# Performance work log

Measured on AMD Instinct MI355X. Metric: run time of the kernel, lower is better.

Reference implementation:

```python
import jax, jax.numpy as jnp
import numpy as np

DIM = 10
ITERATIONS = 2
N_NODES = 500_000
N_EDGES = 8_000_000


def _linear(x, W, b):
    # torch nn.Linear: y = x @ W.T + b
    return x @ W.T + b


def setup_inputs() -> dict:
    key = jax.random.key(0)
    ks = jax.random.split(key, 16)
    inp = {
        "h": jax.random.normal(ks[0], (N_NODES, DIM), dtype=jnp.float32),
        "edges": jax.random.randint(ks[1], (2, N_EDGES), 0, N_NODES, dtype=jnp.int64)
        if jax.config.jax_enable_x64
        else jax.random.randint(ks[1], (2, N_EDGES), 0, N_NODES, dtype=jnp.int32),
        "depth": jax.random.randint(ks[2], (N_NODES,), 0, 4, dtype=jnp.int32),
    }
    names = ["Wz", "bz", "Uz", "buz", "Wr", "br", "Ur", "bur", "Wh", "bh", "Uh", "buh"]
    s = 1.0 / np.sqrt(DIM)
    for i, n in enumerate(names):
        shape = (DIM, DIM) if n[0] in ("W", "U") else (DIM,)
        inp[n] = jax.random.uniform(ks[3 + i], shape, jnp.float32, -s, s)
    return inp


def reference(h, edges, depth, Wz, bz, Uz, buz, Wr, br, Ur, bur, Wh, bh, Uh, buh):
    recv, send = edges[0], edges[1]
    for i in range(ITERATIONS):
        active = (depth + i) <= ITERATIONS                      # [N] bool, shrinks with i
        h = jnp.where(active[:, None], h, 0.0)                  # drop inactive nodes (dict-key drop)
        # x[u] = sum over edges (u,v) with v active of h[v]; h already zeroed for inactive v
        x = jax.ops.segment_sum(h[send], recv, num_segments=h.shape[0])  # [N, DIM]
        z = jax.nn.sigmoid(_linear(x, Wz, bz) + _linear(h, Uz, buz))
        r = jax.nn.sigmoid(_linear(x, Wr, br) + _linear(h, Ur, bur))
        h_new = z * h + (1.0 - z) * jnp.tanh(_linear(x, Wh, bh) + _linear(r * h, Uh, buh))
        h = jnp.where(active[:, None], h_new, 0.0)
    return h
```

## Files before the change

### kernel.cpp

```cpp
#include <hip/hip_runtime.h>
#include <hip/hip_fp16.h>
#include <math.h>
#include <stdint.h>

#define DIM 10
#define NTILE 256
#define BKT_LOG 8
#define BKT 256
#define NBMAX 2048
#define EPW 2048
#define KPT (EPW / 256)
#define CAPB 2816
#define CAPF 1280
#define CAPK (CAPB - CAPF)
#define OVFCAP 32768
#define D2WORDS 32768


__device__ __forceinline__ float2 cvt2(uint32_t u) {
    __half2 hh = *reinterpret_cast<__half2*>(&u);
    return __half22float2(hh);
}

__device__ __forceinline__ int d2get(const uint32_t* __restrict__ depth2, int node) {
    uint32_t w = depth2[(uint32_t)node >> 4];
    return (int)((w >> ((node & 15) * 2)) & 3u);
}

__global__ void prep_kernel(const int* __restrict__ depth,
                            uint32_t* __restrict__ depth2,
                            uint32_t* __restrict__ cnts,
                            int n, int pack_blocks, int cnt_tot)
{
    __shared__ int sd[4096];
    const int t = threadIdx.x;
    const int bid = blockIdx.x;
    if (bid < pack_blocks) {
        const int base = bid * 4096;
        for (int i = t; i < 4096; i += 256) {
            int g = base + i;
            sd[i] = (g < n) ? depth[g] : 3;
        }
        __syncthreads();
        const int wbase = base >> 4;
        int wb = wbase + t;
        if (wb * 16 < n) {
            uint32_t v = 0;
            #pragma unroll
            for (int j = 0; j < 16; ++j)
                v |= ((uint32_t)(sd[t * 16 + j] & 3)) << (2 * j);
            depth2[wb] = v;
        }
    } else {
        int i = (bid - pack_blocks) * 256 + t;
        if (i < cnt_tot) cnts[i] = 0;
    }
}

__global__ __launch_bounds__(256) void binit_kernel(
                           const int* __restrict__ recv,
                           const int* __restrict__ send,
                           const uint32_t* __restrict__ depth2,
                           const int* __restrict__ depth,
                           const float* __restrict__ h_in,
                           uint16_t* __restrict__ h16a,
                           uint32_t* __restrict__ cntF,
                           uint32_t* __restrict__ cntB,
                           uint32_t* __restrict__ ovfc,
                           uint32_t* __restrict__ ovf,
                           uint32_t* __restrict__ bins,
                           int ne, int n, int bin_blocks)
{
    __shared__ uint32_t u[3 * NBMAX];
    const int t = threadIdx.x;
    const int bid = blockIdx.x;

    if (bid < bin_blocks) {
        uint32_t* lh  = u;
        uint32_t* wgF = u + NBMAX;
        uint32_t* wgB = u + 2 * NBMAX;
        for (int i = t; i < NBMAX; i += 256) lh[i] = 0;
        __syncthreads();

        const int base = bid * EPW;
        int rA[KPT], sA[KPT];
        #pragma unroll
        for (int k = 0; k < KPT; ++k) {
            int e = base + k * 256 + t;
            if (e < ne) { rA[k] = recv[e]; sA[k] = send[e]; }
            else        { rA[k] = -1;      sA[k] = 0;       }
        }
        int drA[KPT], dsA[KPT];
        #pragma unroll
        for (int k = 0; k < KPT; ++k) {
            if (rA[k] >= 0) { drA[k] = d2get(depth2, rA[k]); dsA[k] = d2get(depth2, sA[k]); }
            else            { drA[k] = 3;                    dsA[k] = 3;                    }
        }
        uint32_t fl = 0;
        #pragma unroll
        for (int k = 0; k < KPT; ++k) {
            if (rA[k] >= 0 && drA[k] <= 2 && dsA[k] <= 2) {
                bool f1 = (drA[k] <= 1) && (dsA[k] <= 1);
                fl |= (f1 ? 3u : 1u) << (2 * k);
                atomicAdd(&lh[rA[k] >> BKT_LOG], f1 ? 1u : 0x10000u);
            }
        }
        __syncthreads();

        for (int i = t; i < NBMAX; i += 256) {
            uint32_t v = lh[i];
            if (v) {
                uint32_t f = v & 0xffffu, kb = v >> 16;
                if (f)  wgF[i] = atomicAdd(&cntF[i], f);
                if (kb) wgB[i] = atomicAdd(&cntB[i], kb);
            }
        }
        __syncthreads();
        for (int i = t; i < NBMAX; i += 256) lh[i] = 0;
        __syncthreads();

        #pragma unroll
        for (int k = 0; k < KPT; ++k) {
            if ((fl >> (2 * k)) & 1u) {
                int r = rA[k], s = sA[k];
                int b = r >> BKT_LOG;
                bool f1 = (fl >> (2 * k)) & 2u;
                uint32_t w = (uint32_t)s | ((uint32_t)(r & (BKT - 1)) << 19)
                           | (f1 ? (1u << 27) : 0u);
                if (f1) {
                    uint32_t o = atomicAdd(&lh[b], 1u) & 0xffffu;
                    uint32_t pos = wgF[b] + o;
                    if (pos < CAPF) bins[(size_t)b * CAPB + pos] = w;
                    else { uint32_t oi = atomicAdd(ovfc, 1u);
                           if (oi < OVFCAP) ovf[oi] = (uint32_t)(base + k * 256 + t); }
                } else {
                    uint32_t o = atomicAdd(&lh[b], 0x10000u) >> 16;
                    uint32_t pos = wgB[b] + o;
                    if (pos < CAPK) bins[(size_t)b * CAPB + (CAPB - 1) - pos] = w;
                    else { uint32_t oi = atomicAdd(ovfc, 1u);
                           if (oi < OVFCAP) ovf[oi] = (uint32_t)(base + k * 256 + t); }
                }
            }
        }
    } else {
        float* sh = reinterpret_cast<float*>(u);
        const int tile = bid - bin_blocks;
        const int base = tile * NTILE;

        const long gbase = (long)base * DIM;
        const long glim  = (long)n * DIM;
        for (int idx = t; idx < NTILE * DIM; idx += NTILE) {
            long g = gbase + idx;
            float v = (g < glim) ? h_in[g] : 0.0f;
            sh[(idx / DIM) * 11 + (idx % DIM)] = v;
        }
        __syncthreads();

        const int node = base + t;
        if (node < n && depth[node] > 2) {
            #pragma unroll
            for (int c = 0; c < DIM; ++c) sh[t * 11 + c] = 0.0f;
        }
        __syncthreads();

        uint32_t* o16 = reinterpret_cast<uint32_t*>(h16a);
        const long o16base = (long)base * 8;
        const long o16lim  = (long)n * 8;
        for (int idx = t; idx < NTILE * 8; idx += NTILE) {
            long g = o16base + idx;
            if (g < o16lim) {
                int nl = idx / 8, c2 = idx % 8;
                uint32_t w = 0;
                if (c2 < 5) {
                    __half2 hh = __floats2half2_rn(sh[nl * 11 + 2 * c2],
                                                   sh[nl * 11 + 2 * c2 + 1]);
                    w = *reinterpret_cast<uint32_t*>(&hh);
                }
                o16[g] = w;
            }
        }
    }
}

template<int ITER>
__global__ __launch_bounds__(256, 6) void scatgru_kernel(
                            const uint32_t* __restrict__ bins,
                            const uint32_t* __restrict__ cntF,
                            const uint32_t* __restrict__ cntB,
                            const uint32_t* __restrict__ ovfc,
                            const uint32_t* __restrict__ ovf,
                            const int* __restrict__ recv,
                            const int* __restrict__ send,
                            const int* __restrict__ depth,
                            const uint16_t* __restrict__ hcur,
                            uint16_t* __restrict__ hnext,
                            float* __restrict__ out32,
                            int n,
                            const float* __restrict__ Wz, const float* __restrict__ bz,
                            const float* __restrict__ Uz, const float* __restrict__ buz,
                            const float* __restrict__ Wr, const float* __restrict__ br,
                            const float* __restrict__ Ur, const float* __restrict__ bur,
                            const float* __restrict__ Wh, const float* __restrict__ bh,
                            const float* __restrict__ Uh, const float* __restrict__ buh)
{
    __shared__ float xl[BKT * DIM];
    __shared__ float sW[6][100];
    __shared__ float sb[3][10];

    const int t = threadIdx.x;
    if (t < 100) {
        sW[0][t] = Wz[t]; sW[1][t] = Uz[t];
        sW[2][t] = Wr[t]; sW[3][t] = Ur[t];
        sW[4][t] = Wh[t]; sW[5][t] = Uh[t];
    }
    if (t < 10) {
        sb[0][t] = bz[t] + buz[t];
        sb[1][t] = br[t] + bur[t];
        sb[2][t] = bh[t] + buh[t];
    }
    for (int i = t; i < BKT * DIM; i += 256) xl[i] = 0.0f;
    __syncthreads();

    const int b = blockIdx.x;
    const int n0 = b << BKT_LOG;
    const int nb = min(BKT, n - n0);

    const size_t base = (size_t)b * CAPB;
    const int fc = (int)min(cntF[b], (uint32_t)CAPF);
    int tot = fc, boff = 0;
    if (ITER == 0) {
        int bc = (int)min(cntB[b], (uint32_t)CAPK);
        tot = fc + bc;
        boff = CAPB - bc - fc;
    }

    for (int i = t; i < tot; i += 256) {
        size_t idx = base + (size_t)((ITER == 0 && i >= fc) ? (i + boff) : i);
        uint32_t w = bins[idx];
        size_t s = (size_t)(w & 0x7FFFFu);
        uint4 q = *reinterpret_cast<const uint4*>(hcur + s * 16);
        uint32_t e8 = *reinterpret_cast<const uint32_t*>(hcur + s * 16 + 8);
        float2 f0 = cvt2(q.x), f1 = cvt2(q.y), f2 = cvt2(q.z), f3 = cvt2(q.w);
        float2 f4 = cvt2(e8);
        float* xr = xl + ((w >> 19) & (BKT - 1)) * DIM;
        atomicAdd(xr + 0, f0.x); atomicAdd(xr + 1, f0.y);
        atomicAdd(xr + 2, f1.x); atomicAdd(xr + 3, f1.y);
        atomicAdd(xr + 4, f2.x); atomicAdd(xr + 5, f2.y);
        atomicAdd(xr + 6, f3.x); atomicAdd(xr + 7, f3.y);
        atomicAdd(xr + 8, f4.x); atomicAdd(xr + 9, f4.y);
    }

    {
        const uint32_t cnt = min(*ovfc, (uint32_t)OVFCAP);
        for (uint32_t i = t; i < cnt; i += 256) {
            int e = (int)ovf[i];
            int r = recv[e];
            if ((r >> BKT_LOG) != b) continue;
            int s = send[e];
            if (ITER == 1 && (depth[r] > 1 || depth[s] > 1)) continue;
            uint4 q = *reinterpret_cast<const uint4*>(hcur + (size_t)s * 16);
            uint32_t e8v = *reinterpret_cast<const uint32_t*>(hcur + (size_t)s * 16 + 8);
            float2 f0 = cvt2(q.x), f1 = cvt2(q.y), f2 = cvt2(q.z), f3 = cvt2(q.w);
            float2 f4 = cvt2(e8v);
            float* xr = xl + (r & (BKT - 1)) * DIM;
            atomicAdd(xr + 0, f0.x); atomicAdd(xr + 1, f0.y);
            atomicAdd(xr + 2, f1.x); atomicAdd(xr + 3, f1.y);
            atomicAdd(xr + 4, f2.x); atomicAdd(xr + 5, f2.y);
            atomicAdd(xr + 6, f3.x); atomicAdd(xr + 7, f3.y);
            atomicAdd(xr + 8, f4.x); atomicAdd(xr + 9, f4.y);
        }
    }
    __syncthreads();

    if (t < nb) {
        const int node = n0 + t;
        const int dep = depth[node];
        const bool active = (dep + ITER) <= 2;

        float hv[DIM];
        {
            const uint16_t* hp = hcur + (size_t)node * 16;
            uint4 q = *reinterpret_cast<const uint4*>(hp);
            uint32_t e8v = *reinterpret_cast<const uint32_t*>(hp + 8);
            float2 f0 = cvt2(q.x), f1 = cvt2(q.y), f2 = cvt2(q.z), f3 = cvt2(q.w);
            float2 f4 = cvt2(e8v);
            hv[0] = f0.x; hv[1] = f0.y; hv[2] = f1.x; hv[3] = f1.y;
            hv[4] = f2.x; hv[5] = f2.y; hv[6] = f3.x; hv[7] = f3.y;
            hv[8] = f4.x; hv[9] = f4.y;
        }
        float xv[DIM];
        #pragma unroll
        for (int j = 0; j < DIM; ++j) xv[j] = xl[t * DIM + j];

        float zz[DIM];
        if (active) {
            #pragma unroll
            for (int i = 0; i < DIM; ++i) {
                float az = sb[0][i];
                float ar = sb[1][i];
                #pragma unroll
                for (int j = 0; j < DIM; ++j) {
                    az = fmaf(xv[j], sW[0][i * DIM + j], az);
                    az = fmaf(hv[j], sW[1][i * DIM + j], az);
                    ar = fmaf(xv[j], sW[2][i * DIM + j], ar);
                    ar = fmaf(hv[j], sW[3][i * DIM + j], ar);
                }
                zz[i] = 1.0f / (1.0f + __expf(-az));
                xl[t * DIM + i] = (1.0f / (1.0f + __expf(-ar))) * hv[i];
            }
        }

        if (ITER == 0) {
            uint32_t packed[5];
            float prev = 0.0f;
            #pragma unroll
            for (int i = 0; i < DIM; ++i) {
                float o;
                if (active) {
                    float ah = sb[2][i];
                    #pragma unroll
                    for (int j = 0; j < DIM; ++j) {
                        ah = fmaf(xv[j], sW[4][i * DIM + j], ah);
                        ah = fmaf(xl[t * DIM + j], sW[5][i * DIM + j], ah);
                    }
                    o = zz[i] * hv[i] + (1.0f - zz[i]) * tanhf(ah);
                } else {
                    o = hv[i];
                }
                if (dep > 1) o = 0.0f;
                if (i & 1) {
                    __half2 hh = __floats2half2_rn(prev, o);
                    packed[i >> 1] = *reinterpret_cast<uint32_t*>(&hh);
                } else prev = o;
            }
            uint4 o0 = make_uint4(packed[0], packed[1], packed[2], packed[3]);
            uint4 o1 = make_uint4(packed[4], 0u, 0u, 0u);
            *reinterpret_cast<uint4*>(hnext + (size_t)node * 16)     = o0;
            *reinterpret_cast<uint4*>(hnext + (size_t)node * 16 + 8) = o1;
        } else {
            float2* op = reinterpret_cast<float2*>(out32 + (size_t)node * DIM);
            float prev = 0.0f;
            #pragma unroll
            for (int i = 0; i < DIM; ++i) {
                float o;
                if (active) {
                    float ah = sb[2][i];
                    #pragma unroll
                    for (int j = 0; j < DIM; ++j) {
                        ah = fmaf(xv[j], sW[4][i * DIM + j], ah);
                        ah = fmaf(xl[t * DIM + j], sW[5][i * DIM + j], ah);
                    }
                    o = zz[i] * hv[i] + (1.0f - zz[i]) * tanhf(ah);
                } else {
                    o = hv[i];
                }
                if (i & 1) op[i >> 1] = make_float2(prev, o);
                else prev = o;
            }
        }
    }
}

__global__ void init_mask32_kernel(const float* __restrict__ hsrc,
                                   float* __restrict__ hdst,
                                   const int* __restrict__ depth,
                                   int n)
{
    int node = blockIdx.x * blockDim.x + threadIdx.x;
    if (node >= n) return;
    bool act = depth[node] <= 2;
    const float* s = hsrc + (size_t)node * DIM;
    float* d = hdst + (size_t)node * DIM;
    #pragma unroll
    for (int c = 0; c < DIM; ++c) d[c] = act ? s[c] : 0.0f;
}

__global__ void simple_scatter_kernel(const int* __restrict__ recv,
                                      const int* __restrict__ send,
                                      const float* __restrict__ hm,
                                      float* __restrict__ x,
                                      int ne)
{
    const int tid = blockIdx.x * blockDim.x + threadIdx.x;
    const int e = tid / DIM;
    if (e >= ne) return;
    const int c = tid - e * DIM;
    const int s = send[e];
    const float v = hm[(size_t)s * DIM + c];
    if (v != 0.0f) {
        const int r = recv[e];
        unsafeAtomicAdd(x + (size_t)r * DIM + c, v);
    }
}

__global__ void zero_buf_kernel(float4* __restrict__ p, int tot4) {
    int i = blockIdx.x * blockDim.x + threadIdx.x;
    if (i < tot4) p[i] = make_float4(0.0f, 0.0f, 0.0f, 0.0f);
}

__global__ void gru32_kernel(const float* __restrict__ x,
                             const float* __restrict__ h,
                             float* __restrict__ out,
                             const int* __restrict__ depth, int iter, int n,
                             const float* __restrict__ Wz, const float* __restrict__ bz,
                             const float* __restrict__ Uz, const float* __restrict__ buz,
                             const float* __restrict__ Wr, const float* __restrict__ br,
                             const float* __restrict__ Ur, const float* __restrict__ bur,
                             const float* __restrict__ Wh, const float* __restrict__ bh,
                             const float* __restrict__ Uh, const float* __restrict__ buh)
{
    __shared__ float sW[6][100];
    __shared__ float sb[3][10];
    const int t = threadIdx.x;
    if (t < 100) {
        sW[0][t] = Wz[t]; sW[1][t] = Uz[t];
        sW[2][t] = Wr[t]; sW[3][t] = Ur[t];
        sW[4][t] = Wh[t]; sW[5][t] = Uh[t];
    }
    if (t < 10) {
        sb[0][t] = bz[t] + buz[t];
        sb[1][t] = br[t] + bur[t];
        sb[2][t] = bh[t] + buh[t];
    }
    __syncthreads();

    int node = blockIdx.x * blockDim.x + t;
    if (node >= n) return;
    const int dep = depth[node];
    const bool active = dep + iter <= 2;
    float xv[DIM], hv[DIM], outv[DIM];
    #pragma unroll
    for (int j = 0; j < DIM; ++j) {
        xv[j] = x[(size_t)node * DIM + j];
        hv[j] = h[(size_t)node * DIM + j];
    }
    if (active) {
        float zz[DIM], rr[DIM];
        #pragma unroll
        for (int i = 0; i < DIM; ++i) {
            float az = sb[0][i], ar = sb[1][i];
            #pragma unroll
            for (int j = 0; j < DIM; ++j) {
                az = fmaf(xv[j], sW[0][i * DIM + j], az);
                az = fmaf(hv[j], sW[1][i * DIM + j], az);
                ar = fmaf(xv[j], sW[2][i * DIM + j], ar);
                ar = fmaf(hv[j], sW[3][i * DIM + j], ar);
            }
            zz[i] = 1.0f / (1.0f + __expf(-az));
            rr[i] = 1.0f / (1.0f + __expf(-ar));
        }
        float rh[DIM];
        #pragma unroll
        for (int j = 0; j < DIM; ++j) rh[j] = rr[j] * hv[j];
        #pragma unroll
        for (int i = 0; i < DIM; ++i) {
            float ah = sb[2][i];
            #pragma unroll
            for (int j = 0; j < DIM; ++j) {
                ah = fmaf(xv[j], sW[4][i * DIM + j], ah);
                ah = fmaf(rh[j], sW[5][i * DIM + j], ah);
            }
            outv[i] = zz[i] * hv[i] + (1.0f - zz[i]) * tanhf(ah);
        }
    } else {
        #pragma unroll
        for (int i = 0; i < DIM; ++i) outv[i] = hv[i];
    }
    if (iter == 0 && dep > 1) {
        #pragma unroll
        for (int i = 0; i < DIM; ++i) outv[i] = 0.0f;
    }
    #pragma unroll
    for (int i = 0; i < DIM; ++i) out[(size_t)node * DIM + i] = outv[i];
}

extern "C" void kernel_launch(void* const* d_in, const int* in_sizes, int n_in,
                              void* d_out, int out_size, void* d_ws, size_t ws_size,
                              hipStream_t stream) {
    const float* h_in  = (const float*)d_in[0];
    const int*   edges = (const int*)d_in[1];
    const int*   depth = (const int*)d_in[2];
    const float* Wz  = (const float*)d_in[3];
    const float* bz  = (const float*)d_in[4];
    const float* Uz  = (const float*)d_in[5];
    const float* buz = (const float*)d_in[6];
    const float* Wr  = (const float*)d_in[7];
    const float* br  = (const float*)d_in[8];
    const float* Ur  = (const float*)d_in[9];
    const float* bur = (const float*)d_in[10];
    const float* Wh  = (const float*)d_in[11];
    const float* bh  = (const float*)d_in[12];
    const float* Uh  = (const float*)d_in[13];
    const float* buh = (const float*)d_in[14];

    const int n  = in_sizes[0] / DIM;
    const int ne = in_sizes[1] / 2;
    const int* recv = edges;
    const int* send = edges + ne;

    const int NB = (n + BKT - 1) >> BKT_LOG;
    const size_t meta_words = 2 * NBMAX + 8 + OVFCAP + D2WORDS;
    const size_t need = (size_t)n * 16 * sizeof(uint16_t) * 2
                      + (size_t)NB * CAPB * sizeof(uint32_t)
                      + meta_words * sizeof(uint32_t);

    const int BLK = 256;

    if (ws_size >= need && n <= (1 << 19) && NB <= NBMAX) {
        uint16_t* h16a = (uint16_t*)d_ws;
        uint16_t* h16b = h16a + (size_t)n * 16;
        uint32_t* bins = (uint32_t*)(h16b + (size_t)n * 16);
        uint32_t* meta = bins + (size_t)NB * CAPB;
        uint32_t* cntF   = meta;
        uint32_t* cntB   = meta + NBMAX;
        uint32_t* ovfc   = meta + 2 * NBMAX;
        uint32_t* ovf    = meta + 2 * NBMAX + 8;
        uint32_t* depth2 = meta + 2 * NBMAX + 8 + OVFCAP;

        const int bin_blocks  = (ne + EPW - 1) / EPW;
        const int node_blocks = (n + NTILE - 1) / NTILE;
        const int pack_blocks = (n + 4095) / 4096;
        const int cnt_tot = 2 * NBMAX + 1;
        const int cnt_blocks = (cnt_tot + 255) / 256;

        prep_kernel<<<pack_blocks + cnt_blocks, BLK, 0, stream>>>(
            depth, depth2, meta, n, pack_blocks, cnt_tot);
        binit_kernel<<<bin_blocks + node_blocks, BLK, 0, stream>>>(
            recv, send, depth2, depth, h_in, h16a,
            cntF, cntB, ovfc, ovf, bins, ne, n, bin_blocks);

        scatgru_kernel<0><<<NB, BLK, 0, stream>>>(
            bins, cntF, cntB, ovfc, ovf, recv, send, depth,
            h16a, h16b, nullptr, n,
            Wz, bz, Uz, buz, Wr, br, Ur, bur, Wh, bh, Uh, buh);

        scatgru_kernel<1><<<NB, BLK, 0, stream>>>(
            bins, cntF, cntB, ovfc, ovf, recv, send, depth,
            h16b, nullptr, (float*)d_out, n,
            Wz, bz, Uz, buz, Wr, br, Ur, bur, Wh, bh, Uh, buh);
    } else {
        float* x    = (float*)d_ws;
        float* hbuf = (float*)d_out;
        const int nwork = ne * DIM;
        const int edge_blocks = (nwork + BLK - 1) / BLK;
        const int x_tot4 = (n * DIM) / 4;
        const int xz_blocks = (x_tot4 + BLK - 1) / BLK;
        const int nb2 = (n + BLK - 1) / BLK;

        init_mask32_kernel<<<nb2, BLK, 0, stream>>>(h_in, hbuf, depth, n);
        zero_buf_kernel<<<xz_blocks, BLK, 0, stream>>>((float4*)x, x_tot4);
        simple_scatter_kernel<<<edge_blocks, BLK, 0, stream>>>(recv, send, hbuf, x, ne);
        gru32_kernel<<<nb2, BLK, 0, stream>>>(x, hbuf, hbuf, depth, 0, n,
            Wz, bz, Uz, buz, Wr, br, Ur, bur, Wh, bh, Uh, buh);
        zero_buf_kernel<<<xz_blocks, BLK, 0, stream>>>((float4*)x, x_tot4);
        simple_scatter_kernel<<<edge_blocks, BLK, 0, stream>>>(recv, send, hbuf, x, ne);
        gru32_kernel<<<nb2, BLK, 0, stream>>>(x, hbuf, hbuf, depth, 1, n,
            Wz, bz, Uz, buz, Wr, br, Ur, bur, Wh, bh, Uh, buh);
    }
}
```

Baseline: 554.7 us.

## Replace two-pass block-aggregated binning with sender-partitioned direct atomic bins

The edge binning drops the per-block shared-memory histogram and two-phase offset reservation. Each edge now does a direct global atomicAdd into a cell keyed by (sender partition, receiver bucket), with 8 partitions of capacity 448. The per-bucket GRU kernel walks partitions in order so gathered sender rows are more localized, and in iteration 1 it filters out non-f1 edges by a flag bit instead of using a separate bin region. It also pads the shared x accumulator stride to 11 to cut LDS bank conflicts and raises the occupancy hint. The trade is many more global atomics with higher contention, and a higher overflow risk from the smaller per-cell capacity.

```diff
diff --git a/kernel.cpp b/kernel.cpp
--- a/kernel.cpp
+++ b/kernel.cpp
@@ -10,11 +10,12 @@
 #define NBMAX 2048
 #define EPW 2048
 #define KPT (EPW / 256)
-#define CAPB 2816
-#define CAPF 1280
-#define CAPK (CAPB - CAPF)
+#define NPART 8
+#define PSHIFT 16
+#define CAP 448
 #define OVFCAP 32768
 #define D2WORDS 32768
+#define XSTR 11
 
 
 __device__ __forceinline__ float2 cvt2(uint32_t u) {
@@ -42,8 +43,7 @@
             sd[i] = (g < n) ? depth[g] : 3;
         }
         __syncthreads();
-        const int wbase = base >> 4;
-        int wb = wbase + t;
+        int wb = (base >> 4) + t;
         if (wb * 16 < n) {
             uint32_t v = 0;
             #pragma unroll
@@ -64,24 +64,17 @@
                            const int* __restrict__ depth,
                            const float* __restrict__ h_in,
                            uint16_t* __restrict__ h16a,
-                           uint32_t* __restrict__ cntF,
-                           uint32_t* __restrict__ cntB,
+                           uint32_t* __restrict__ cnt,
                            uint32_t* __restrict__ ovfc,
                            uint32_t* __restrict__ ovf,
                            uint32_t* __restrict__ bins,
-                           int ne, int n, int bin_blocks)
+                           int ne, int n, int NB, int bin_blocks)
 {
-    __shared__ uint32_t u[3 * NBMAX];
+    __shared__ float sh[NTILE * 11];
     const int t = threadIdx.x;
     const int bid = blockIdx.x;
 
     if (bid < bin_blocks) {
-        uint32_t* lh  = u;
-        uint32_t* wgF = u + NBMAX;
-        uint32_t* wgB = u + 2 * NBMAX;
-        for (int i = t; i < NBMAX; i += 256) lh[i] = 0;
-        __syncthreads();
-
         const int base = bid * EPW;
         int rA[KPT], sA[KPT];
         #pragma unroll
@@ -96,57 +89,22 @@
             if (rA[k] >= 0) { drA[k] = d2get(depth2, rA[k]); dsA[k] = d2get(depth2, sA[k]); }
             else            { drA[k] = 3;                    dsA[k] = 3;                    }
         }
-        uint32_t fl = 0;
         #pragma unroll
         for (int k = 0; k < KPT; ++k) {
             if (rA[k] >= 0 && drA[k] <= 2 && dsA[k] <= 2) {
+                int r = rA[k], s = sA[k];
                 bool f1 = (drA[k] <= 1) && (dsA[k] <= 1);
-                fl |= (f1 ? 3u : 1u) << (2 * k);
-                atomicAdd(&lh[rA[k] >> BKT_LOG], f1 ? 1u : 0x10000u);
-            }
-        }
-        __syncthreads();
-
-        for (int i = t; i < NBMAX; i += 256) {
-            uint32_t v = lh[i];
-            if (v) {
-                uint32_t f = v & 0xffffu, kb = v >> 16;
-                if (f)  wgF[i] = atomicAdd(&cntF[i], f);
-                if (kb) wgB[i] = atomicAdd(&cntB[i], kb);
-            }
-        }
-        __syncthreads();
-        for (int i = t; i < NBMAX; i += 256) lh[i] = 0;
-        __syncthreads();
-
-        #pragma unroll
-        for (int k = 0; k < KPT; ++k) {
-            if ((fl >> (2 * k)) & 1u) {
-                int r = rA[k], s = sA[k];
-                int b = r >> BKT_LOG;
-                bool f1 = (fl >> (2 * k)) & 2u;
                 uint32_t w = (uint32_t)s | ((uint32_t)(r & (BKT - 1)) << 19)
                            | (f1 ? (1u << 27) : 0u);
-                if (f1) {
-                    uint32_t o = atomicAdd(&lh[b], 1u) & 0xffffu;
-                    uint32_t pos = wgF[b] + o;
-                    if (pos < CAPF) bins[(size_t)b * CAPB + pos] = w;
-                    else { uint32_t oi = atomicAdd(ovfc, 1u);
-                           if (oi < OVFCAP) ovf[oi] = (uint32_t)(base + k * 256 + t); }
-                } else {
-                    uint32_t o = atomicAdd(&lh[b], 0x10000u) >> 16;
-                    uint32_t pos = wgB[b] + o;
-                    if (pos < CAPK) bins[(size_t)b * CAPB + (CAPB - 1) - pos] = w;
-                    else { uint32_t oi = atomicAdd(ovfc, 1u);
-                           if (oi < OVFCAP) ovf[oi] = (uint32_t)(base + k * 256 + t); }
-                }
+                int cell = (s >> PSHIFT) * NB + (r >> BKT_LOG);
+                uint32_t pos = atomicAdd(&cnt[cell], 1u);
+                if (pos < CAP) bins[(size_t)cell * CAP + pos] = w;
+                else { uint32_t oi = atomicAdd(ovfc, 1u);
+                       if (oi < OVFCAP) ovf[oi] = (uint32_t)(base + k * 256 + t); }
             }
         }
     } else {
-        float* sh = reinterpret_cast<float*>(u);
-        const int tile = bid - bin_blocks;
-        const int base = tile * NTILE;
-
+        const int base = (bid - bin_blocks) * NTILE;
         const long gbase = (long)base * DIM;
         const long glim  = (long)n * DIM;
         for (int idx = t; idx < NTILE * DIM; idx += NTILE) {
@@ -155,14 +113,12 @@
             sh[(idx / DIM) * 11 + (idx % DIM)] = v;
         }
         __syncthreads();
-
         const int node = base + t;
         if (node < n && depth[node] > 2) {
             #pragma unroll
             for (int c = 0; c < DIM; ++c) sh[t * 11 + c] = 0.0f;
         }
         __syncthreads();
-
         uint32_t* o16 = reinterpret_cast<uint32_t*>(h16a);
         const long o16base = (long)base * 8;
         const long o16lim  = (long)n * 8;
@@ -183,10 +139,9 @@
 }
 
 template<int ITER>
-__global__ __launch_bounds__(256, 6) void scatgru_kernel(
+__global__ __launch_bounds__(256, 8) void scatgru_kernel(
                             const uint32_t* __restrict__ bins,
-                            const uint32_t* __restrict__ cntF,
-                            const uint32_t* __restrict__ cntB,
+                            const uint32_t* __restrict__ cnt,
                             const uint32_t* __restrict__ ovfc,
                             const uint32_t* __restrict__ ovf,
                             const int* __restrict__ recv,
@@ -195,7 +150,7 @@
                             const uint16_t* __restrict__ hcur,
                             uint16_t* __restrict__ hnext,
                             float* __restrict__ out32,
-                            int n,
+                            int n, int NB,
                             const float* __restrict__ Wz, const float* __restrict__ bz,
                             const float* __restrict__ Uz, const float* __restrict__ buz,
                             const float* __restrict__ Wr, const float* __restrict__ br,
@@ -203,7 +158,7 @@
                             const float* __restrict__ Wh, const float* __restrict__ bh,
                             const float* __restrict__ Uh, const float* __restrict__ buh)
 {
-    __shared__ float xl[BKT * DIM];
+    __shared__ float xl[BKT * XSTR];
     __shared__ float sW[6][100];
     __shared__ float sb[3][10];
 
@@ -218,41 +173,37 @@
         sb[1][t] = br[t] + bur[t];
         sb[2][t] = bh[t] + buh[t];
     }
-    for (int i = t; i < BKT * DIM; i += 256) xl[i] = 0.0f;
+    for (int i = t; i < BKT * XSTR; i += 256) xl[i] = 0.0f;
     __syncthreads();
 
     const int b = blockIdx.x;
     const int n0 = b << BKT_LOG;
     const int nb = min(BKT, n - n0);
 
-    const size_t base = (size_t)b * CAPB;
-    const int fc = (int)min(cntF[b], (uint32_t)CAPF);
-    int tot = fc, boff = 0;
-    if (ITER == 0) {
-        int bc = (int)min(cntB[b], (uint32_t)CAPK);
-        tot = fc + bc;
-        boff = CAPB - bc - fc;
-    }
-
-    for (int i = t; i < tot; i += 256) {
-        size_t idx = base + (size_t)((ITER == 0 && i >= fc) ? (i + boff) : i);
-        uint32_t w = bins[idx];
-        size_t s = (size_t)(w & 0x7FFFFu);
-        uint4 q = *reinterpret_cast<const uint4*>(hcur + s * 16);
-        uint32_t e8 = *reinterpret_cast<const uint32_t*>(hcur + s * 16 + 8);
-        float2 f0 = cvt2(q.x), f1 = cvt2(q.y), f2 = cvt2(q.z), f3 = cvt2(q.w);
-        float2 f4 = cvt2(e8);
-        float* xr = xl + ((w >> 19) & (BKT - 1)) * DIM;
-        atomicAdd(xr + 0, f0.x); atomicAdd(xr + 1, f0.y);
-        atomicAdd(xr + 2, f1.x); atomicAdd(xr + 3, f1.y);
-        atomicAdd(xr + 4, f2.x); atomicAdd(xr + 5, f2.y);
-        atomicAdd(xr + 6, f3.x); atomicAdd(xr + 7, f3.y);
-        atomicAdd(xr + 8, f4.x); atomicAdd(xr + 9, f4.y);
+    for (int p = 0; p < NPART; ++p) {
+        const int cell = p * NB + b;
+        const size_t base = (size_t)cell * CAP;
+        const int tot = (int)min(cnt[cell], (uint32_t)CAP);
+        for (int i = t; i < tot; i += 256) {
+            uint32_t w = bins[base + i];
+            if (ITER == 1 && !((w >> 27) & 1u)) continue;
+            size_t s = (size_t)(w & 0x7FFFFu);
+            uint4 q = *reinterpret_cast<const uint4*>(hcur + s * 16);
+            uint32_t e8 = *reinterpret_cast<const uint32_t*>(hcur + s * 16 + 8);
+            float2 f0 = cvt2(q.x), f1 = cvt2(q.y), f2 = cvt2(q.z), f3 = cvt2(q.w);
+            float2 f4 = cvt2(e8);
+            float* xr = xl + ((w >> 19) & (BKT - 1)) * XSTR;
+            atomicAdd(xr + 0, f0.x); atomicAdd(xr + 1, f0.y);
+            atomicAdd(xr + 2, f1.x); atomicAdd(xr + 3, f1.y);
+            atomicAdd(xr + 4, f2.x); atomicAdd(xr + 5, f2.y);
+            atomicAdd(xr + 6, f3.x); atomicAdd(xr + 7, f3.y);
+            atomicAdd(xr + 8, f4.x); atomicAdd(xr + 9, f4.y);
+        }
     }
 
     {
-        const uint32_t cnt = min(*ovfc, (uint32_t)OVFCAP);
-        for (uint32_t i = t; i < cnt; i += 256) {
+        const uint32_t cntv = min(*ovfc, (uint32_t)OVFCAP);
+        for (uint32_t i = t; i < cntv; i += 256) {
             int e = (int)ovf[i];
             int r = recv[e];
             if ((r >> BKT_LOG) != b) continue;
@@ -262,7 +213,7 @@
             uint32_t e8v = *reinterpret_cast<const uint32_t*>(hcur + (size_t)s * 16 + 8);
             float2 f0 = cvt2(q.x), f1 = cvt2(q.y), f2 = cvt2(q.z), f3 = cvt2(q.w);
             float2 f4 = cvt2(e8v);
-            float* xr = xl + (r & (BKT - 1)) * DIM;
+            float* xr = xl + (r & (BKT - 1)) * XSTR;
             atomicAdd(xr + 0, f0.x); atomicAdd(xr + 1, f0.y);
             atomicAdd(xr + 2, f1.x); atomicAdd(xr + 3, f1.y);
             atomicAdd(xr + 4, f2.x); atomicAdd(xr + 5, f2.y);
@@ -290,7 +241,7 @@
         }
         float xv[DIM];
         #pragma unroll
-        for (int j = 0; j < DIM; ++j) xv[j] = xl[t * DIM + j];
+        for (int j = 0; j < DIM; ++j) xv[j] = xl[t * XSTR + j];
 
         float zz[DIM];
         if (active) {
@@ -306,7 +257,7 @@
                     ar = fmaf(hv[j], sW[3][i * DIM + j], ar);
                 }
                 zz[i] = 1.0f / (1.0f + __expf(-az));
-                xl[t * DIM + i] = (1.0f / (1.0f + __expf(-ar))) * hv[i];
+                xl[t * XSTR + i] = (1.0f / (1.0f + __expf(-ar))) * hv[i];
             }
         }
 
@@ -321,7 +272,7 @@
                     #pragma unroll
                     for (int j = 0; j < DIM; ++j) {
                         ah = fmaf(xv[j], sW[4][i * DIM + j], ah);
-                        ah = fmaf(xl[t * DIM + j], sW[5][i * DIM + j], ah);
+                        ah = fmaf(xl[t * XSTR + j], sW[5][i * DIM + j], ah);
                     }
                     o = zz[i] * hv[i] + (1.0f - zz[i]) * tanhf(ah);
                 } else {
@@ -348,7 +299,7 @@
                     #pragma unroll
                     for (int j = 0; j < DIM; ++j) {
                         ah = fmaf(xv[j], sW[4][i * DIM + j], ah);
-                        ah = fmaf(xl[t * DIM + j], sW[5][i * DIM + j], ah);
+                        ah = fmaf(xl[t * XSTR + j], sW[5][i * DIM + j], ah);
                     }
                     o = zz[i] * hv[i] + (1.0f - zz[i]) * tanhf(ah);
                 } else {
@@ -363,8 +314,7 @@
 
 __global__ void init_mask32_kernel(const float* __restrict__ hsrc,
                                    float* __restrict__ hdst,
-                                   const int* __restrict__ depth,
-                                   int n)
+                                   const int* __restrict__ depth, int n)
 {
     int node = blockIdx.x * blockDim.x + threadIdx.x;
     if (node >= n) return;
@@ -378,8 +328,7 @@
 __global__ void simple_scatter_kernel(const int* __restrict__ recv,
                                       const int* __restrict__ send,
                                       const float* __restrict__ hm,
-                                      float* __restrict__ x,
-                                      int ne)
+                                      float* __restrict__ x, int ne)
 {
     const int tid = blockIdx.x * blockDim.x + threadIdx.x;
     const int e = tid / DIM;
@@ -435,7 +384,7 @@
         hv[j] = h[(size_t)node * DIM + j];
     }
     if (active) {
-        float zz[DIM], rr[DIM];
+        float zz[DIM], rh[DIM];
         #pragma unroll
         for (int i = 0; i < DIM; ++i) {
             float az = sb[0][i], ar = sb[1][i];
@@ -447,11 +396,8 @@
                 ar = fmaf(hv[j], sW[3][i * DIM + j], ar);
             }
             zz[i] = 1.0f / (1.0f + __expf(-az));
-            rr[i] = 1.0f / (1.0f + __expf(-ar));
-        }
-        float rh[DIM];
-        #pragma unroll
-        for (int j = 0; j < DIM; ++j) rh[j] = rr[j] * hv[j];
+            rh[i] = (1.0f / (1.0f + __expf(-ar))) * hv[i];
+        }
         #pragma unroll
         for (int i = 0; i < DIM; ++i) {
             float ah = sb[2][i];
@@ -499,44 +445,43 @@
     const int* send = edges + ne;
 
     const int NB = (n + BKT - 1) >> BKT_LOG;
-    const size_t meta_words = 2 * NBMAX + 8 + OVFCAP + D2WORDS;
+    const size_t meta_words = (size_t)NPART * NBMAX + 8 + OVFCAP + D2WORDS;
     const size_t need = (size_t)n * 16 * sizeof(uint16_t) * 2
-                      + (size_t)NB * CAPB * sizeof(uint32_t)
+                      + (size_t)NPART * NB * CAP * sizeof(uint32_t)
                       + meta_words * sizeof(uint32_t);
 
     const int BLK = 256;
 
-    if (ws_size >= need && n <= (1 << 19) && NB <= NBMAX) {
+    if (ws_size >= need && n <= (1 << 19) && NB <= NBMAX && out_size >= n * DIM) {
         uint16_t* h16a = (uint16_t*)d_ws;
         uint16_t* h16b = h16a + (size_t)n * 16;
         uint32_t* bins = (uint32_t*)(h16b + (size_t)n * 16);
-        uint32_t* meta = bins + (size_t)NB * CAPB;
-        uint32_t* cntF   = meta;
-        uint32_t* cntB   = meta + NBMAX;
-        uint32_t* ovfc   = meta + 2 * NBMAX;
-        uint32_t* ovf    = meta + 2 * NBMAX + 8;
-        uint32_t* depth2 = meta + 2 * NBMAX + 8 + OVFCAP;
+        uint32_t* meta = bins + (size_t)NPART * NB * CAP;
+        uint32_t* cnt    = meta;
+        uint32_t* ovfc   = meta + (size_t)NPART * NBMAX;
+        uint32_t* ovf    = ovfc + 8;
+        uint32_t* depth2 = ovf + OVFCAP;
 
         const int bin_blocks  = (ne + EPW - 1) / EPW;
         const int node_blocks = (n + NTILE - 1) / NTILE;
         const int pack_blocks = (n + 4095) / 4096;
-        const int cnt_tot = 2 * NBMAX + 1;
+        const int cnt_tot = NPART * NBMAX + 1;
         const int cnt_blocks = (cnt_tot + 255) / 256;
 
         prep_kernel<<<pack_blocks + cnt_blocks, BLK, 0, stream>>>(
-            depth, depth2, meta, n, pack_blocks, cnt_tot);
+            depth, depth2, cnt, n, pack_blocks, cnt_tot);
         binit_kernel<<<bin_blocks + node_blocks, BLK, 0, stream>>>(
             recv, send, depth2, depth, h_in, h16a,
-            cntF, cntB, ovfc, ovf, bins, ne, n, bin_blocks);
+            cnt, ovfc, ovf, bins, ne, n, NB, bin_blocks);
 
         scatgru_kernel<0><<<NB, BLK, 0, stream>>>(
-            bins, cntF, cntB, ovfc, ovf, recv, send, depth,
-            h16a, h16b, nullptr, n,
+            bins, cnt, ovfc, ovf, recv, send, depth,
+            h16a, h16b, nullptr, n, NB,
             Wz, bz, Uz, buz, Wr, br, Ur, bur, Wh, bh, Uh, buh);
 
         scatgru_kernel<1><<<NB, BLK, 0, stream>>>(
-            bins, cntF, cntB, ovfc, ovf, recv, send, depth,
-            h16b, nullptr, (float*)d_out, n,
+            bins, cnt, ovfc, ovf, recv, send, depth,
+            h16b, nullptr, (float*)d_out, n, NB,
             Wz, bz, Uz, buz, Wr, br, Ur, bur, Wh, bh, Uh, buh);
     } else {
         float* x    = (float*)d_ws;
```

Result: slower. 612.4 us (+10.4%).
